# Optimization experiments

Measured on AMD Instinct MI355X. Metric: run time of the kernel, lower is better.

Reference implementation:

```python
import jax, jax.numpy as jnp
import numpy as np

T, OBS, H, NOBJ = 32768, 256, 512, 4


def _xavier(key, shape):
    fan_in, fan_out = shape[0], shape[1]
    lim = jnp.sqrt(6.0 / (fan_in + fan_out)).astype(jnp.float32)
    return jax.random.uniform(key, shape, jnp.float32, -lim, lim)


def setup_inputs() -> dict:
    key = jax.random.key(0)
    ks = jax.random.split(key, 16)
    # weights stored as [in, out] so y = x @ W (same math as nn.Linear with W.T)
    return {
        "x": jax.random.normal(ks[0], (T, OBS), jnp.float32),
        "W_in0": _xavier(ks[1], (OBS, H)),
        "W_B0": _xavier(ks[2], (OBS, H)),
        "W_C0": _xavier(ks[3], (OBS, H)),
        "W_d0": _xavier(ks[4], (OBS, H)),
        "A_log0": jax.random.normal(ks[5], (H,), jnp.float32),
        "W_in1": _xavier(ks[6], (H, H)),
        "W_B1": _xavier(ks[7], (H, H)),
        "W_C1": _xavier(ks[8], (H, H)),
        "W_d1": _xavier(ks[9], (H, H)),
        "A_log1": jax.random.normal(ks[10], (H,), jnp.float32),
        "W_out": _xavier(ks[11], (H, NOBJ)),
        "b_out": jnp.zeros((NOBJ,), jnp.float32),
        "W_skip": _xavier(ks[12], (OBS, NOBJ)),
    }


def _mamba_layer(x, W_in, W_B, W_C, W_d, A_log):
    # x: [T, D_in] -> [T, H]
    x_state = x @ W_in           # [T, H]
    B = x @ W_B                  # [T, H]
    C = x @ W_C                  # [T, H]
    delta = jax.nn.sigmoid(x @ W_d)  # [T, H]
    A = -jnp.exp(A_log)          # [H]
    A_bar = jnp.exp(delta * A)   # [T, H], in (0, 1)
    Bx = B * x_state             # [T, H]

    def step(h, inp):
        a_t, bx_t = inp
        h = a_t * h + bx_t
        return h, h

    h0 = jnp.zeros((x_state.shape[-1],), x_state.dtype)
    _, h_seq = jax.lax.scan(step, h0, (A_bar, Bx))  # [T, H]
    return C * h_seq


def reference(x, W_in0, W_B0, W_C0, W_d0, A_log0,
              W_in1, W_B1, W_C1, W_d1, A_log1,
              W_out, b_out, W_skip):
    skip = x
    y = _mamba_layer(x, W_in0, W_B0, W_C0, W_d0, A_log0)
    y = _mamba_layer(y, W_in1, W_B1, W_C1, W_d1, A_log1)
    out = y @ W_out + b_out + skip @ W_skip  # [T, NOBJ]
    return out
```

## Files before the change

### kernel.cpp

```cpp
#include <hip/hip_runtime.h>

typedef __attribute__((ext_vector_type(8))) short short8;
typedef __attribute__((ext_vector_type(4))) float floatx4;

#define T_SIZE 32768
#define OBS    256
#define H      512
#define NC     1024
#define CHUNK  32
#define NGRP   64
#define GCH    16
#define SLAB   ((size_t)T_SIZE * 32)

__device__ __forceinline__ unsigned short f2bf(float f){
    union { float f; unsigned u; } v; v.f = f;
    unsigned u = v.u;
    u += 0x7FFFu + ((u >> 16) & 1u);
    return (unsigned short)(u >> 16);
}
__device__ __forceinline__ float bf2f(unsigned short u){
    union { unsigned u; float f; } v; v.u = ((unsigned)u) << 16; return v.f;
}

#define GLOAD_LDS16(g, l) \
    __builtin_amdgcn_global_load_lds((const __attribute__((address_space(1))) unsigned*)(g), \
                                     (__attribute__((address_space(3))) unsigned*)(l), 16, 0, 0)

__global__ void cast_x_kernel(const float* __restrict__ x, unsigned short* __restrict__ xb, int n4){
    int i = blockIdx.x * 256 + threadIdx.x;
    if (i < n4){
        float4 v = ((const float4*)x)[i];
        ushort4 o;
        o.x = f2bf(v.x); o.y = f2bf(v.y); o.z = f2bf(v.z); o.w = f2bf(v.w);
        ((ushort4*)xb)[i] = o;
    }
}

__global__ void tcast4_kernel(const float* __restrict__ W0, const float* __restrict__ W1,
                              const float* __restrict__ W2, const float* __restrict__ W3,
                              unsigned short* __restrict__ dst, int K, int KH){
    int idx = blockIdx.x * 256 + threadIdx.x;
    if (idx >= 4 * KH) return;
    int s   = idx / KH;
    int rem = idx - s * KH;
    int k = rem >> 9;
    int h = rem & 511;
    const float* W = (s == 0) ? W0 : (s == 1) ? W1 : (s == 2) ? W2 : W3;
    int b = h >> 4, hh = h & 15;
    dst[(size_t)((b * 4 + s) * 16 + hh) * K + k] = f2bf(W[(size_t)k * H + h]);
}

template<int K>
__global__ __launch_bounds__(256) void gemm_layer_kernel(
    const unsigned short* __restrict__ xb,
    const unsigned short* __restrict__ wt,
    const float* __restrict__ A_log,
    unsigned short* __restrict__ gT, unsigned short* __restrict__ bxT, unsigned short* __restrict__ CT,
    float* __restrict__ Pbuf, float* __restrict__ Hbuf)
{
    __shared__ unsigned short SM[4][8192];

    const int tid  = threadIdx.x;
    const int wave = tid >> 6;
    const int lane = tid & 63;
    const int ml   = lane & 15;
    const int quad = lane >> 4;
    const int wm   = wave & 1;
    const int wn   = wave >> 1;

    const int flat = blockIdx.y * 16 + blockIdx.x;
    const int xcd  = flat & 7;
    const int j    = flat >> 3;
    const int nb   = j & 15;
    const int mb   = (j >> 4) * 8 + xcd;
    const int m0   = mb * 128;

    const int srow = tid >> 2;
    const int sel  = (((tid & 3) ^ ((tid >> 3) & 3))) * 8;
    const int swz  = (ml >> 1) & 3;

    const unsigned short* pa0 = xb + (size_t)(m0 + srow) * K + sel;
    const unsigned short* pa1 = pa0 + (size_t)64 * K;
    const unsigned short* pb0 = wt + (size_t)(nb * 128 + srow) * K + sel;
    const unsigned short* pb1 = pb0 + (size_t)64 * K;

    const int ldsA0 = (wave * 64 + 0  ) * 8;
    const int ldsA1 = (wave * 64 + 256) * 8;

    const int rbaseA = (wm * 64 + ml) * 32 + (quad ^ swz) * 8;
    const int rbaseB = (wn * 64 + ml) * 32 + (quad ^ swz) * 8;

    floatx4 acc[4][4];
    #pragma unroll
    for (int i = 0; i < 4; i++)
        #pragma unroll
        for (int jj = 0; jj < 4; jj++)
            acc[i][jj] = (floatx4)(0.0f);

    constexpr int NK = K >> 5;

    #pragma unroll
    for (int p = 0; p < 3; ++p){
        const int ko = p * 32;
        GLOAD_LDS16(pa0 + ko, &SM[p][ldsA0]);
        GLOAD_LDS16(pa1 + ko, &SM[p][ldsA1]);
        GLOAD_LDS16(pb0 + ko, &SM[p][4096 + ldsA0]);
        GLOAD_LDS16(pb1 + ko, &SM[p][4096 + ldsA1]);
    }
    asm volatile("s_waitcnt vmcnt(8)" ::: "memory");
    __builtin_amdgcn_s_barrier();
    __builtin_amdgcn_sched_barrier(0);

    #pragma unroll
    for (int kk = 0; kk < NK; ++kk){
        const int cur = kk & 3;

        if (kk + 3 < NK){
            const int ko  = (kk + 3) * 32;
            const int nb4 = (kk + 3) & 3;
            GLOAD_LDS16(pa0 + ko, &SM[nb4][ldsA0]);
            GLOAD_LDS16(pa1 + ko, &SM[nb4][ldsA1]);
            GLOAD_LDS16(pb0 + ko, &SM[nb4][4096 + ldsA0]);
            GLOAD_LDS16(pb1 + ko, &SM[nb4][4096 + ldsA1]);
        }

        short8 av[4], bv[4];
        #pragma unroll
        for (int i = 0; i < 4; i++)
            av[i] = *(const short8*)(&SM[cur][0] + rbaseA + i * 16 * 32);
        #pragma unroll
        for (int jj = 0; jj < 4; jj++)
            bv[jj] = *(const short8*)(&SM[cur][4096] + rbaseB + jj * 16 * 32);

        __builtin_amdgcn_s_setprio(1);
        #pragma unroll
        for (int i = 0; i < 4; i++)
            #pragma unroll
            for (int jj = 0; jj < 4; jj++)
                acc[i][jj] = __builtin_amdgcn_mfma_f32_16x16x32_bf16(av[i], bv[jj], acc[i][jj], 0, 0, 0);
        __builtin_amdgcn_s_setprio(0);

        if (kk + 1 < NK){
            const int hi = (kk + 3 < NK) ? (kk + 3) : (NK - 1);
            const int vm = 4 * (hi - (kk + 1));
            if (vm >= 8)      asm volatile("s_waitcnt vmcnt(8)" ::: "memory");
            else if (vm == 4) asm volatile("s_waitcnt vmcnt(4)" ::: "memory");
            else              asm volatile("s_waitcnt vmcnt(0)" ::: "memory");
            __builtin_amdgcn_s_barrier();
            __builtin_amdgcn_sched_barrier(0);
        }
    }
    __syncthreads();

    unsigned short* SMe = &SM[0][0];
    float2* segbuf = (float2*)(SMe + 12288);
    const int col = wn * 16 + ml;
    const int h   = nb * 32 + col;
    const float Aneg = -expf(A_log[h]);

    #pragma unroll
    for (int i = 0; i < 4; i++){
        float p = 1.0f, hh = 0.0f;
        #pragma unroll
        for (int r = 0; r < 4; r++){
            int trow = wm * 64 + i * 16 + quad * 4 + r;
            float dv = acc[i][3][r];
            float delta = 1.0f / (1.0f + expf(-dv));
            unsigned short gb = f2bf(delta * Aneg);
            float a = expf(bf2f(gb));
            unsigned short bb = f2bf(acc[i][1][r] * acc[i][0][r]);
            SMe[        trow * 32 + col] = gb;
            SMe[4096 +  trow * 32 + col] = bb;
            SMe[8192 +  trow * 32 + col] = f2bf(acc[i][2][r]);
            hh = fmaf(a, hh, bf2f(bb));
            p *= a;
        }
        const int ch = wm * 2 + (i >> 1);
        const int s  = (i & 1) * 4 + quad;
        segbuf[(ch * 8 + s) * 32 + col] = make_float2(p, hh);
    }
    __syncthreads();
    {
        const short8* s8 = (const short8*)SMe;
        short8* dg = (short8*)(gT  + (size_t)nb * SLAB + (size_t)m0 * 32);
        short8* db = (short8*)(bxT + (size_t)nb * SLAB + (size_t)m0 * 32);
        short8* dc = (short8*)(CT  + (size_t)nb * SLAB + (size_t)m0 * 32);
        dg[tid] = s8[tid];        dg[tid + 256] = s8[tid + 256];
        db[tid] = s8[512 + tid];  db[tid + 256] = s8[768 + tid];
        dc[tid] = s8[1024 + tid]; dc[tid + 256] = s8[1280 + tid];
    }
    if (tid < 128){
        const int ccol = tid & 31, ch = tid >> 5;
        float P = 1.0f, Hc = 0.0f;
        #pragma unroll
        for (int s = 0; s < 8; s++){
            float2 ph = segbuf[(ch * 8 + s) * 32 + ccol];
            Hc = fmaf(ph.x, Hc, ph.y);
            P *= ph.x;
        }
        const int c = mb * 4 + ch;
        Pbuf[(size_t)c * H + nb * 32 + ccol] = P;
        Hbuf[(size_t)c * H + nb * 32 + ccol] = Hc;
    }
}

__global__ void scan2a_kernel(const float* __restrict__ P, const float* __restrict__ Hc,
                              float* __restrict__ Pg, float* __restrict__ Hg){
    const int g  = blockIdx.x;
    const int j4 = threadIdx.x * 4;
    float4 pc = {1.f,1.f,1.f,1.f}, hc = {0.f,0.f,0.f,0.f};
    #pragma unroll
    for (int i = 0; i < GCH; i++){
        size_t o = (size_t)(g * GCH + i) * H + j4;
        float4 P4 = *(const float4*)(P + o);
        float4 H4 = *(const float4*)(Hc + o);
        hc.x = fmaf(P4.x, hc.x, H4.x); pc.x *= P4.x;
        hc.y = fmaf(P4.y, hc.y, H4.y); pc.y *= P4.y;
        hc.z = fmaf(P4.z, hc.z, H4.z); pc.z *= P4.z;
        hc.w = fmaf(P4.w, hc.w, H4.w); pc.w *= P4.w;
    }
    *(float4*)(Pg + (size_t)g * H + j4) = pc;
    *(float4*)(Hg + (size_t)g * H + j4) = hc;
}

__global__ void scan2b_kernel(const float* __restrict__ Pg, const float* __restrict__ Hg,
                              float* __restrict__ Cg){
    const int j = threadIdx.x;
    float carry = 0.0f;
    for (int g0 = 0; g0 < NGRP; g0 += 8){
        float p[8], h[8];
        #pragma unroll
        for (int i = 0; i < 8; i++){
            p[i] = Pg[(size_t)(g0 + i) * H + j];
            h[i] = Hg[(size_t)(g0 + i) * H + j];
        }
        #pragma unroll
        for (int i = 0; i < 8; i++){
            Cg[(size_t)(g0 + i) * H + j] = carry;
            carry = fmaf(p[i], carry, h[i]);
        }
    }
}

__global__ void scan3_kernel(const unsigned short* __restrict__ gT, const unsigned short* __restrict__ bxT,
                             const unsigned short* __restrict__ CT,
                             const float* __restrict__ P, const float* __restrict__ Hc,
                             const float* __restrict__ Cg,
                             unsigned short* __restrict__ yb){
    int idx = blockIdx.x * 256 + threadIdx.x;
    int j4 = (idx & 127) * 4;
    int c  = idx >> 7;
    int nb = j4 >> 5, jj = j4 & 31;
    int grp = c >> 4;
    float4 h = *(const float4*)(Cg + (size_t)grp * H + j4);
    for (int cc = grp << 4; cc < c; ++cc){
        float4 P4 = *(const float4*)(P + (size_t)cc * H + j4);
        float4 H4 = *(const float4*)(Hc + (size_t)cc * H + j4);
        h.x = fmaf(P4.x, h.x, H4.x);
        h.y = fmaf(P4.y, h.y, H4.y);
        h.z = fmaf(P4.z, h.z, H4.z);
        h.w = fmaf(P4.w, h.w, H4.w);
    }
    size_t off = (size_t)nb * SLAB + (size_t)c * CHUNK * 32 + jj;
    size_t yo  = (size_t)c * CHUNK * H + j4;
    #pragma unroll 8
    for (int i = 0; i < CHUNK; i++){
        ushort4 gv = *(const ushort4*)(gT + off);
        ushort4 bv = *(const ushort4*)(bxT + off);
        ushort4 cv = *(const ushort4*)(CT + off);
        h.x = fmaf(expf(bf2f(gv.x)), h.x, bf2f(bv.x));
        h.y = fmaf(expf(bf2f(gv.y)), h.y, bf2f(bv.y));
        h.z = fmaf(expf(bf2f(gv.z)), h.z, bf2f(bv.z));
        h.w = fmaf(expf(bf2f(gv.w)), h.w, bf2f(bv.w));
        ushort4 o;
        o.x = f2bf(bf2f(cv.x) * h.x);
        o.y = f2bf(bf2f(cv.y) * h.y);
        o.z = f2bf(bf2f(cv.z) * h.z);
        o.w = f2bf(bf2f(cv.w) * h.w);
        *(ushort4*)(yb + yo) = o;
        off += 32; yo += H;
    }
}

__global__ __launch_bounds__(256) void final_kernel(const unsigned short* __restrict__ y2,
                                                    const unsigned short* __restrict__ xb,
                                                    const float* __restrict__ Wout,
                                                    const float* __restrict__ bout,
                                                    const float* __restrict__ Wskip,
                                                    float* __restrict__ out){
    int wave = threadIdx.x >> 6;
    int lane = threadIdx.x & 63;
    int t = blockIdx.x * 4 + wave;
    float s0 = 0.f, s1 = 0.f, s2 = 0.f, s3 = 0.f;
    const float4* W4 = (const float4*)Wout;
    #pragma unroll
    for (int k = lane; k < H; k += 64){
        float yv = bf2f(y2[(size_t)t * H + k]);
        float4 w = W4[k];
        s0 = fmaf(yv, w.x, s0); s1 = fmaf(yv, w.y, s1);
        s2 = fmaf(yv, w.z, s2); s3 = fmaf(yv, w.w, s3);
    }
    const float4* S4 = (const float4*)Wskip;
    #pragma unroll
    for (int k = lane; k < OBS; k += 64){
        float xv = bf2f(xb[(size_t)t * OBS + k]);
        float4 w = S4[k];
        s0 = fmaf(xv, w.x, s0); s1 = fmaf(xv, w.y, s1);
        s2 = fmaf(xv, w.z, s2); s3 = fmaf(xv, w.w, s3);
    }
    #pragma unroll
    for (int off = 32; off > 0; off >>= 1){
        s0 += __shfl_down(s0, off);
        s1 += __shfl_down(s1, off);
        s2 += __shfl_down(s2, off);
        s3 += __shfl_down(s3, off);
    }
    if (lane == 0){
        out[(size_t)t * 4 + 0] = s0 + bout[0];
        out[(size_t)t * 4 + 1] = s1 + bout[1];
        out[(size_t)t * 4 + 2] = s2 + bout[2];
        out[(size_t)t * 4 + 3] = s3 + bout[3];
    }
}

extern "C" void kernel_launch(void* const* d_in, const int* in_sizes, int n_in,
                              void* d_out, int out_size, void* d_ws, size_t ws_size,
                              hipStream_t stream)
{
    const float* x     = (const float*)d_in[0];
    const float* W_in0 = (const float*)d_in[1];
    const float* W_B0  = (const float*)d_in[2];
    const float* W_C0  = (const float*)d_in[3];
    const float* W_d0  = (const float*)d_in[4];
    const float* A0    = (const float*)d_in[5];
    const float* W_in1 = (const float*)d_in[6];
    const float* W_B1  = (const float*)d_in[7];
    const float* W_C1  = (const float*)d_in[8];
    const float* W_d1  = (const float*)d_in[9];
    const float* A1    = (const float*)d_in[10];
    const float* Wout  = (const float*)d_in[11];
    const float* bout  = (const float*)d_in[12];
    const float* Wskip = (const float*)d_in[13];
    float* out = (float*)d_out;

    char* ws = (char*)d_ws;
    size_t off = 0;
    auto alloc = [&](size_t bytes) -> void* {
        void* p = ws + off;
        off += (bytes + 255) & ~(size_t)255;
        return p;
    };
    unsigned short* xb  = (unsigned short*)alloc((size_t)T_SIZE * OBS * 2);
    unsigned short* yb  = (unsigned short*)alloc((size_t)T_SIZE * H * 2);
    unsigned short* Wt0 = (unsigned short*)alloc((size_t)4 * H * OBS * 2);
    unsigned short* Wt1 = (unsigned short*)alloc((size_t)4 * H * H * 2);
    unsigned short* gT  = (unsigned short*)alloc((size_t)T_SIZE * H * 2);
    unsigned short* bxT = (unsigned short*)alloc((size_t)T_SIZE * H * 2);
    unsigned short* CT  = (unsigned short*)alloc((size_t)T_SIZE * H * 2);
    float* Pbuf = (float*)alloc((size_t)NC * H * 4);
    float* Hbuf = (float*)alloc((size_t)NC * H * 4);
    float* Pg   = (float*)alloc((size_t)NGRP * H * 4);
    float* Hg   = (float*)alloc((size_t)NGRP * H * 4);
    float* Cg   = (float*)alloc((size_t)NGRP * H * 4);
    (void)ws_size; (void)in_sizes; (void)n_in; (void)out_size;

    cast_x_kernel<<<(T_SIZE * OBS / 4 + 255) / 256, 256, 0, stream>>>(x, xb, T_SIZE * OBS / 4);
    tcast4_kernel<<<(4 * OBS * H + 255) / 256, 256, 0, stream>>>(W_in0, W_B0, W_C0, W_d0, Wt0, OBS, OBS * H);
    tcast4_kernel<<<(4 * H   * H + 255) / 256, 256, 0, stream>>>(W_in1, W_B1, W_C1, W_d1, Wt1, H,   H * H);

    dim3 ggrid(16, 256);
    const int sgrid = NC * 128 / 256;

    gemm_layer_kernel<OBS><<<ggrid, 256, 0, stream>>>(xb, Wt0, A0, gT, bxT, CT, Pbuf, Hbuf);
    scan2a_kernel<<<NGRP, 128, 0, stream>>>(Pbuf, Hbuf, Pg, Hg);
    scan2b_kernel<<<1, H, 0, stream>>>(Pg, Hg, Cg);
    scan3_kernel<<<sgrid, 256, 0, stream>>>(gT, bxT, CT, Pbuf, Hbuf, Cg, yb);

    gemm_layer_kernel<H><<<ggrid, 256, 0, stream>>>(yb, Wt1, A1, gT, bxT, CT, Pbuf, Hbuf);
    scan2a_kernel<<<NGRP, 128, 0, stream>>>(Pbuf, Hbuf, Pg, Hg);
    scan2b_kernel<<<1, H, 0, stream>>>(Pg, Hg, Cg);
    scan3_kernel<<<sgrid, 256, 0, stream>>>(gT, bxT, CT, Pbuf, Hbuf, Cg, yb );

    final_kernel<<<T_SIZE / 4, 256, 0, stream>>>(yb, xb, Wout, bout, Wskip, out);
}
```

Baseline: 334.2 us.

## Enlarge GEMM tile to 256x256 with 8 waves and split-phase prefetch

Doubles the fused projection GEMM block tile from 128x128 to 256x256 using 512 threads. Each wave now computes 128x64, and each K-step is split into two MFMA halves, with the A and B prefetches for the stage three steps ahead interleaved between the halves. The goal is more operand reuse per byte loaded and fewer blocks. The epilogue is reworked so one block writes two 32-column slabs and eight chunk summaries. The trade-off is 128 KB of shared memory and more accumulator registers, which limits occupancy, plus extra barriers per K-step.

```diff
diff --git a/kernel.cpp b/kernel.cpp
--- a/kernel.cpp
+++ b/kernel.cpp
@@ -51,156 +51,176 @@
 }
 
 template<int K>
-__global__ __launch_bounds__(256) void gemm_layer_kernel(
+__global__ __launch_bounds__(512, 2) void gemm_layer_kernel(
     const unsigned short* __restrict__ xb,
     const unsigned short* __restrict__ wt,
     const float* __restrict__ A_log,
     unsigned short* __restrict__ gT, unsigned short* __restrict__ bxT, unsigned short* __restrict__ CT,
     float* __restrict__ Pbuf, float* __restrict__ Hbuf)
 {
-    __shared__ unsigned short SM[4][8192];
+    __shared__ unsigned short SM[4][16384];
 
     const int tid  = threadIdx.x;
     const int wave = tid >> 6;
     const int lane = tid & 63;
     const int ml   = lane & 15;
     const int quad = lane >> 4;
-    const int wm   = wave & 1;
-    const int wn   = wave >> 1;
-
-    const int flat = blockIdx.y * 16 + blockIdx.x;
+    const int wm   = wave >> 2;
+    const int wn   = wave & 3;
+
+    const int flat = blockIdx.y * 8 + blockIdx.x;
     const int xcd  = flat & 7;
     const int j    = flat >> 3;
-    const int nb   = j & 15;
-    const int mb   = (j >> 4) * 8 + xcd;
-    const int m0   = mb * 128;
+    const int nb   = j & 7;
+    const int mb   = (j >> 3) * 8 + xcd;
+    const int m0   = mb * 256;
 
     const int srow = tid >> 2;
-    const int sel  = (((tid & 3) ^ ((tid >> 3) & 3))) * 8;
+    const int sel  = ((tid & 3) ^ ((tid >> 3) & 3)) * 8;
     const int swz  = (ml >> 1) & 3;
 
     const unsigned short* pa0 = xb + (size_t)(m0 + srow) * K + sel;
-    const unsigned short* pa1 = pa0 + (size_t)64 * K;
-    const unsigned short* pb0 = wt + (size_t)(nb * 128 + srow) * K + sel;
-    const unsigned short* pb1 = pb0 + (size_t)64 * K;
-
-    const int ldsA0 = (wave * 64 + 0  ) * 8;
-    const int ldsA1 = (wave * 64 + 256) * 8;
-
-    const int rbaseA = (wm * 64 + ml) * 32 + (quad ^ swz) * 8;
-    const int rbaseB = (wn * 64 + ml) * 32 + (quad ^ swz) * 8;
-
-    floatx4 acc[4][4];
-    #pragma unroll
-    for (int i = 0; i < 4; i++)
-        #pragma unroll
-        for (int jj = 0; jj < 4; jj++)
-            acc[i][jj] = (floatx4)(0.0f);
+    const unsigned short* pa1 = pa0 + (size_t)128 * K;
+    const unsigned short* pb0 = wt + (size_t)(nb * 256 + srow) * K + sel;
+    const unsigned short* pb1 = pb0 + (size_t)128 * K;
+
+    const int ldsA0 = wave * 512;
+    const int ldsA1 = 4096  + wave * 512;
+    const int ldsB0 = 8192  + wave * 512;
+    const int ldsB1 = 12288 + wave * 512;
+
+    const int rbaseA = (wm * 128 + ml) * 32 + (quad ^ swz) * 8;
+    const int rbaseB = (wn * 64  + ml) * 32 + (quad ^ swz) * 8;
+
+    floatx4 acc[8][4];
+    #pragma unroll
+    for (int m = 0; m < 8; m++)
+        #pragma unroll
+        for (int n = 0; n < 4; n++)
+            acc[m][n] = (floatx4)(0.0f);
 
     constexpr int NK = K >> 5;
 
-    #pragma unroll
-    for (int p = 0; p < 3; ++p){
-        const int ko = p * 32;
-        GLOAD_LDS16(pa0 + ko, &SM[p][ldsA0]);
-        GLOAD_LDS16(pa1 + ko, &SM[p][ldsA1]);
-        GLOAD_LDS16(pb0 + ko, &SM[p][4096 + ldsA0]);
-        GLOAD_LDS16(pb1 + ko, &SM[p][4096 + ldsA1]);
-    }
+#define STAGE_A(kt_) { const int b_ = (kt_) & 3; const int ko_ = (kt_) * 32; \
+        GLOAD_LDS16(pa0 + ko_, &SM[b_][ldsA0]); \
+        GLOAD_LDS16(pa1 + ko_, &SM[b_][ldsA1]); }
+#define STAGE_B(kt_) { const int b_ = (kt_) & 3; const int ko_ = (kt_) * 32; \
+        GLOAD_LDS16(pb0 + ko_, &SM[b_][ldsB0]); \
+        GLOAD_LDS16(pb1 + ko_, &SM[b_][ldsB1]); }
+
+    STAGE_A(0); STAGE_B(0);
+    STAGE_A(1); STAGE_B(1);
+    STAGE_A(2); STAGE_B(2);
     asm volatile("s_waitcnt vmcnt(8)" ::: "memory");
     __builtin_amdgcn_s_barrier();
     __builtin_amdgcn_sched_barrier(0);
 
     #pragma unroll
-    for (int kk = 0; kk < NK; ++kk){
-        const int cur = kk & 3;
-
-        if (kk + 3 < NK){
-            const int ko  = (kk + 3) * 32;
-            const int nb4 = (kk + 3) & 3;
-            GLOAD_LDS16(pa0 + ko, &SM[nb4][ldsA0]);
-            GLOAD_LDS16(pa1 + ko, &SM[nb4][ldsA1]);
-            GLOAD_LDS16(pb0 + ko, &SM[nb4][4096 + ldsA0]);
-            GLOAD_LDS16(pb1 + ko, &SM[nb4][4096 + ldsA1]);
-        }
+    for (int kt = 0; kt < NK; ++kt){
+        const unsigned short* SA = &SM[kt & 3][0];
+        const unsigned short* SB = SA + 8192;
 
         short8 av[4], bv[4];
         #pragma unroll
-        for (int i = 0; i < 4; i++)
-            av[i] = *(const short8*)(&SM[cur][0] + rbaseA + i * 16 * 32);
-        #pragma unroll
-        for (int jj = 0; jj < 4; jj++)
-            bv[jj] = *(const short8*)(&SM[cur][4096] + rbaseB + jj * 16 * 32);
-
+        for (int m = 0; m < 4; m++) av[m] = *(const short8*)(SA + rbaseA + m * 512);
+        #pragma unroll
+        for (int n = 0; n < 4; n++) bv[n] = *(const short8*)(SB + rbaseB + n * 512);
+        if (kt + 3 < NK) STAGE_A(kt + 3);
+        __builtin_amdgcn_s_barrier();
+        asm volatile("s_waitcnt lgkmcnt(0)" ::: "memory");
+        __builtin_amdgcn_sched_barrier(0);
         __builtin_amdgcn_s_setprio(1);
         #pragma unroll
-        for (int i = 0; i < 4; i++)
+        for (int m = 0; m < 4; m++)
             #pragma unroll
-            for (int jj = 0; jj < 4; jj++)
-                acc[i][jj] = __builtin_amdgcn_mfma_f32_16x16x32_bf16(av[i], bv[jj], acc[i][jj], 0, 0, 0);
+            for (int n = 0; n < 4; n++)
+                acc[m][n] = __builtin_amdgcn_mfma_f32_16x16x32_bf16(av[m], bv[n], acc[m][n], 0, 0, 0);
         __builtin_amdgcn_s_setprio(0);
-
-        if (kk + 1 < NK){
-            const int hi = (kk + 3 < NK) ? (kk + 3) : (NK - 1);
-            const int vm = 4 * (hi - (kk + 1));
-            if (vm >= 8)      asm volatile("s_waitcnt vmcnt(8)" ::: "memory");
-            else if (vm == 4) asm volatile("s_waitcnt vmcnt(4)" ::: "memory");
-            else              asm volatile("s_waitcnt vmcnt(0)" ::: "memory");
-            __builtin_amdgcn_s_barrier();
-            __builtin_amdgcn_sched_barrier(0);
-        }
+        __builtin_amdgcn_s_barrier();
+        __builtin_amdgcn_sched_barrier(0);
+
+        short8 aw[4];
+        #pragma unroll
+        for (int m = 0; m < 4; m++) aw[m] = *(const short8*)(SA + rbaseA + (m + 4) * 512);
+        if (kt + 3 < NK) STAGE_B(kt + 3);
+        __builtin_amdgcn_s_barrier();
+        asm volatile("s_waitcnt lgkmcnt(0)" ::: "memory");
+        __builtin_amdgcn_sched_barrier(0);
+        __builtin_amdgcn_s_setprio(1);
+        #pragma unroll
+        for (int m = 0; m < 4; m++)
+            #pragma unroll
+            for (int n = 0; n < 4; n++)
+                acc[m + 4][n] = __builtin_amdgcn_mfma_f32_16x16x32_bf16(aw[m], bv[n], acc[m + 4][n], 0, 0, 0);
+        __builtin_amdgcn_s_setprio(0);
+        if (kt + 1 < NK){
+            if (kt + 3 < NK)       { asm volatile("s_waitcnt vmcnt(8)" ::: "memory"); }
+            else if (kt + 3 == NK) { asm volatile("s_waitcnt vmcnt(4)" ::: "memory"); }
+            else                   { asm volatile("s_waitcnt vmcnt(0)" ::: "memory"); }
+        }
+        __builtin_amdgcn_s_barrier();
+        __builtin_amdgcn_sched_barrier(0);
     }
     __syncthreads();
 
+#undef STAGE_A
+#undef STAGE_B
+
     unsigned short* SMe = &SM[0][0];
-    float2* segbuf = (float2*)(SMe + 12288);
-    const int col = wn * 16 + ml;
-    const int h   = nb * 32 + col;
-    const float Aneg = -expf(A_log[h]);
-
-    #pragma unroll
-    for (int i = 0; i < 4; i++){
+    float2* segbuf = (float2*)(SMe + 49152);
+    const int hcol  = wn * 16 + ml;
+    const int hb    = wn >> 1;
+    const int col32 = (wn & 1) * 16 + ml;
+    const float Aneg = -expf(A_log[(nb * 4 + wn) * 16 + ml]);
+
+    #pragma unroll
+    for (int m = 0; m < 8; m++){
         float p = 1.0f, hh = 0.0f;
         #pragma unroll
         for (int r = 0; r < 4; r++){
-            int trow = wm * 64 + i * 16 + quad * 4 + r;
-            float dv = acc[i][3][r];
+            int trow = wm * 128 + m * 16 + quad * 4 + r;
+            float dv = acc[m][3][r];
             float delta = 1.0f / (1.0f + expf(-dv));
             unsigned short gb = f2bf(delta * Aneg);
             float a = expf(bf2f(gb));
-            unsigned short bb = f2bf(acc[i][1][r] * acc[i][0][r]);
-            SMe[        trow * 32 + col] = gb;
-            SMe[4096 +  trow * 32 + col] = bb;
-            SMe[8192 +  trow * 32 + col] = f2bf(acc[i][2][r]);
+            unsigned short bb = f2bf(acc[m][1][r] * acc[m][0][r]);
+            int base = hb * 8192 + trow * 32 + col32;
+            SMe[        base] = gb;
+            SMe[16384 + base] = bb;
+            SMe[32768 + base] = f2bf(acc[m][2][r]);
             hh = fmaf(a, hh, bf2f(bb));
             p *= a;
         }
-        const int ch = wm * 2 + (i >> 1);
-        const int s  = (i & 1) * 4 + quad;
-        segbuf[(ch * 8 + s) * 32 + col] = make_float2(p, hh);
+        const int ch = wm * 4 + (m >> 1);
+        const int s  = (m & 1) * 4 + quad;
+        segbuf[(ch * 8 + s) * 64 + hcol] = make_float2(p, hh);
     }
     __syncthreads();
     {
         const short8* s8 = (const short8*)SMe;
-        short8* dg = (short8*)(gT  + (size_t)nb * SLAB + (size_t)m0 * 32);
-        short8* db = (short8*)(bxT + (size_t)nb * SLAB + (size_t)m0 * 32);
-        short8* dc = (short8*)(CT  + (size_t)nb * SLAB + (size_t)m0 * 32);
-        dg[tid] = s8[tid];        dg[tid + 256] = s8[tid + 256];
-        db[tid] = s8[512 + tid];  db[tid + 256] = s8[768 + tid];
-        dc[tid] = s8[1024 + tid]; dc[tid + 256] = s8[1280 + tid];
-    }
-    if (tid < 128){
-        const int ccol = tid & 31, ch = tid >> 5;
+        #pragma unroll
+        for (int arr = 0; arr < 3; arr++){
+            unsigned short* bp = (arr == 0) ? gT : (arr == 1) ? bxT : CT;
+            #pragma unroll
+            for (int h2 = 0; h2 < 2; h2++){
+                short8* d = (short8*)(bp + (size_t)(nb * 2 + h2) * SLAB + (size_t)m0 * 32);
+                d[tid]       = s8[arr * 2048 + h2 * 1024 + tid];
+                d[tid + 512] = s8[arr * 2048 + h2 * 1024 + tid + 512];
+            }
+        }
+    }
+    {
+        const int ccol = tid & 63, ch = tid >> 6;
         float P = 1.0f, Hc = 0.0f;
         #pragma unroll
         for (int s = 0; s < 8; s++){
-            float2 ph = segbuf[(ch * 8 + s) * 32 + ccol];
+            float2 ph = segbuf[(ch * 8 + s) * 64 + ccol];
             Hc = fmaf(ph.x, Hc, ph.y);
             P *= ph.x;
         }
-        const int c = mb * 4 + ch;
-        Pbuf[(size_t)c * H + nb * 32 + ccol] = P;
-        Hbuf[(size_t)c * H + nb * 32 + ccol] = Hc;
+        const int c = mb * 8 + ch;
+        Pbuf[(size_t)c * H + nb * 64 + ccol] = P;
+        Hbuf[(size_t)c * H + nb * 64 + ccol] = Hc;
     }
 }
 
@@ -368,15 +388,15 @@
     tcast4_kernel<<<(4 * OBS * H + 255) / 256, 256, 0, stream>>>(W_in0, W_B0, W_C0, W_d0, Wt0, OBS, OBS * H);
     tcast4_kernel<<<(4 * H   * H + 255) / 256, 256, 0, stream>>>(W_in1, W_B1, W_C1, W_d1, Wt1, H,   H * H);
 
-    dim3 ggrid(16, 256);
+    dim3 ggrid(8, 128);
     const int sgrid = NC * 128 / 256;
 
-    gemm_layer_kernel<OBS><<<ggrid, 256, 0, stream>>>(xb, Wt0, A0, gT, bxT, CT, Pbuf, Hbuf);
+    gemm_layer_kernel<OBS><<<ggrid, 512, 0, stream>>>(xb, Wt0, A0, gT, bxT, CT, Pbuf, Hbuf);
     scan2a_kernel<<<NGRP, 128, 0, stream>>>(Pbuf, Hbuf, Pg, Hg);
     scan2b_kernel<<<1, H, 0, stream>>>(Pg, Hg, Cg);
     scan3_kernel<<<sgrid, 256, 0, stream>>>(gT, bxT, CT, Pbuf, Hbuf, Cg, yb);
 
-    gemm_layer_kernel<H><<<ggrid, 256, 0, stream>>>(yb, Wt1, A1, gT, bxT, CT, Pbuf, Hbuf);
+    gemm_layer_kernel<H><<<ggrid, 512, 0, stream>>>(yb, Wt1, A1, gT, bxT, CT, Pbuf, Hbuf);
     scan2a_kernel<<<NGRP, 128, 0, stream>>>(Pbuf, Hbuf, Pg, Hg);
     scan2b_kernel<<<1, H, 0, stream>>>(Pg, Hg, Cg);
     scan3_kernel<<<sgrid, 256, 0, stream>>>(gT, bxT, CT, Pbuf, Hbuf, Cg, yb );
```

Result: no change. 336.0 us (+0.6%).

## Fuse prep casts, drop group-carry scan kernel, fuse final projection into scan

Applied to the files above, without the earlier changes.

Merges the x cast and both weight transpose-casts into one prep launch. Removes the serial single-block scan2b kernel by having each scan3 thread recompute its group carry from the group prefix arrays, which costs up to 63 extra float4 steps per thread. The last layer's scan is fused with the output projection: each block stages its 64 output rows in LDS (64 KB) and computes the 4-wide dot products directly, so the second-layer y buffer is never written to or read back from global memory. That shared-memory use may cut occupancy for the fused kernel.

```diff
diff --git a/kernel.cpp b/kernel.cpp
--- a/kernel.cpp
+++ b/kernel.cpp
@@ -26,28 +26,42 @@
     __builtin_amdgcn_global_load_lds((const __attribute__((address_space(1))) unsigned*)(g), \
                                      (__attribute__((address_space(3))) unsigned*)(l), 16, 0, 0)
 
-__global__ void cast_x_kernel(const float* __restrict__ x, unsigned short* __restrict__ xb, int n4){
-    int i = blockIdx.x * 256 + threadIdx.x;
-    if (i < n4){
+__global__ void prep_kernel(const float* __restrict__ x, unsigned short* __restrict__ xb,
+                            const float* __restrict__ A0W0, const float* __restrict__ A0W1,
+                            const float* __restrict__ A0W2, const float* __restrict__ A0W3,
+                            unsigned short* __restrict__ Wt0,
+                            const float* __restrict__ A1W0, const float* __restrict__ A1W1,
+                            const float* __restrict__ A1W2, const float* __restrict__ A1W3,
+                            unsigned short* __restrict__ Wt1){
+    const int b = blockIdx.x;
+    const int tid = threadIdx.x;
+    if (b < 8192){
+        int i = b * 256 + tid;
         float4 v = ((const float4*)x)[i];
         ushort4 o;
         o.x = f2bf(v.x); o.y = f2bf(v.y); o.z = f2bf(v.z); o.w = f2bf(v.w);
         ((ushort4*)xb)[i] = o;
-    }
-}
-
-__global__ void tcast4_kernel(const float* __restrict__ W0, const float* __restrict__ W1,
-                              const float* __restrict__ W2, const float* __restrict__ W3,
-                              unsigned short* __restrict__ dst, int K, int KH){
-    int idx = blockIdx.x * 256 + threadIdx.x;
-    if (idx >= 4 * KH) return;
-    int s   = idx / KH;
-    int rem = idx - s * KH;
-    int k = rem >> 9;
-    int h = rem & 511;
-    const float* W = (s == 0) ? W0 : (s == 1) ? W1 : (s == 2) ? W2 : W3;
-    int b = h >> 4, hh = h & 15;
-    dst[(size_t)((b * 4 + s) * 16 + hh) * K + k] = f2bf(W[(size_t)k * H + h]);
+    } else if (b < 10240){
+        const int K = OBS, KH = OBS * H;
+        int idx = (b - 8192) * 256 + tid;
+        int s   = idx / KH;
+        int rem = idx - s * KH;
+        int k = rem >> 9;
+        int h = rem & 511;
+        const float* W = (s == 0) ? A0W0 : (s == 1) ? A0W1 : (s == 2) ? A0W2 : A0W3;
+        int bb = h >> 4, hh = h & 15;
+        Wt0[(size_t)((bb * 4 + s) * 16 + hh) * K + k] = f2bf(W[(size_t)k * H + h]);
+    } else {
+        const int K = H, KH = H * H;
+        int idx = (b - 10240) * 256 + tid;
+        int s   = idx / KH;
+        int rem = idx - s * KH;
+        int k = rem >> 9;
+        int h = rem & 511;
+        const float* W = (s == 0) ? A1W0 : (s == 1) ? A1W1 : (s == 2) ? A1W2 : A1W3;
+        int bb = h >> 4, hh = h & 15;
+        Wt1[(size_t)((bb * 4 + s) * 16 + hh) * K + k] = f2bf(W[(size_t)k * H + h]);
+    }
 }
 
 template<int K>
@@ -223,36 +237,25 @@
     *(float4*)(Hg + (size_t)g * H + j4) = hc;
 }
 
-__global__ void scan2b_kernel(const float* __restrict__ Pg, const float* __restrict__ Hg,
-                              float* __restrict__ Cg){
-    const int j = threadIdx.x;
-    float carry = 0.0f;
-    for (int g0 = 0; g0 < NGRP; g0 += 8){
-        float p[8], h[8];
-        #pragma unroll
-        for (int i = 0; i < 8; i++){
-            p[i] = Pg[(size_t)(g0 + i) * H + j];
-            h[i] = Hg[(size_t)(g0 + i) * H + j];
-        }
-        #pragma unroll
-        for (int i = 0; i < 8; i++){
-            Cg[(size_t)(g0 + i) * H + j] = carry;
-            carry = fmaf(p[i], carry, h[i]);
-        }
-    }
-}
-
 __global__ void scan3_kernel(const unsigned short* __restrict__ gT, const unsigned short* __restrict__ bxT,
                              const unsigned short* __restrict__ CT,
                              const float* __restrict__ P, const float* __restrict__ Hc,
-                             const float* __restrict__ Cg,
+                             const float* __restrict__ Pg, const float* __restrict__ Hg,
                              unsigned short* __restrict__ yb){
     int idx = blockIdx.x * 256 + threadIdx.x;
     int j4 = (idx & 127) * 4;
     int c  = idx >> 7;
     int nb = j4 >> 5, jj = j4 & 31;
     int grp = c >> 4;
-    float4 h = *(const float4*)(Cg + (size_t)grp * H + j4);
+    float4 h = {0.f, 0.f, 0.f, 0.f};
+    for (int g = 0; g < grp; ++g){
+        float4 P4 = *(const float4*)(Pg + (size_t)g * H + j4);
+        float4 H4 = *(const float4*)(Hg + (size_t)g * H + j4);
+        h.x = fmaf(P4.x, h.x, H4.x);
+        h.y = fmaf(P4.y, h.y, H4.y);
+        h.z = fmaf(P4.z, h.z, H4.z);
+        h.w = fmaf(P4.w, h.w, H4.w);
+    }
     for (int cc = grp << 4; cc < c; ++cc){
         float4 P4 = *(const float4*)(P + (size_t)cc * H + j4);
         float4 H4 = *(const float4*)(Hc + (size_t)cc * H + j4);
@@ -282,44 +285,96 @@
     }
 }
 
-__global__ __launch_bounds__(256) void final_kernel(const unsigned short* __restrict__ y2,
-                                                    const unsigned short* __restrict__ xb,
-                                                    const float* __restrict__ Wout,
-                                                    const float* __restrict__ bout,
-                                                    const float* __restrict__ Wskip,
-                                                    float* __restrict__ out){
-    int wave = threadIdx.x >> 6;
-    int lane = threadIdx.x & 63;
-    int t = blockIdx.x * 4 + wave;
-    float s0 = 0.f, s1 = 0.f, s2 = 0.f, s3 = 0.f;
+__global__ __launch_bounds__(256) void scan3f_kernel(
+    const unsigned short* __restrict__ gT, const unsigned short* __restrict__ bxT,
+    const unsigned short* __restrict__ CT,
+    const float* __restrict__ P, const float* __restrict__ Hc,
+    const float* __restrict__ Pg, const float* __restrict__ Hg,
+    const unsigned short* __restrict__ xb,
+    const float* __restrict__ Wout, const float* __restrict__ bout,
+    const float* __restrict__ Wskip,
+    float* __restrict__ out){
+    __shared__ unsigned short ystage[64 * 512];
+    const int tid = threadIdx.x;
+    int idx = blockIdx.x * 256 + tid;
+    int j4 = (idx & 127) * 4;
+    int c  = idx >> 7;
+    int nb = j4 >> 5, jj = j4 & 31;
+    int grp = c >> 4;
+    float4 h = {0.f, 0.f, 0.f, 0.f};
+    for (int g = 0; g < grp; ++g){
+        float4 P4 = *(const float4*)(Pg + (size_t)g * H + j4);
+        float4 H4 = *(const float4*)(Hg + (size_t)g * H + j4);
+        h.x = fmaf(P4.x, h.x, H4.x);
+        h.y = fmaf(P4.y, h.y, H4.y);
+        h.z = fmaf(P4.z, h.z, H4.z);
+        h.w = fmaf(P4.w, h.w, H4.w);
+    }
+    for (int cc = grp << 4; cc < c; ++cc){
+        float4 P4 = *(const float4*)(P + (size_t)cc * H + j4);
+        float4 H4 = *(const float4*)(Hc + (size_t)cc * H + j4);
+        h.x = fmaf(P4.x, h.x, H4.x);
+        h.y = fmaf(P4.y, h.y, H4.y);
+        h.z = fmaf(P4.z, h.z, H4.z);
+        h.w = fmaf(P4.w, h.w, H4.w);
+    }
+    size_t off = (size_t)nb * SLAB + (size_t)c * CHUNK * 32 + jj;
+    const int lrow = (tid >> 7) * 32;
+    #pragma unroll 8
+    for (int i = 0; i < CHUNK; i++){
+        ushort4 gv = *(const ushort4*)(gT + off);
+        ushort4 bv = *(const ushort4*)(bxT + off);
+        ushort4 cv = *(const ushort4*)(CT + off);
+        h.x = fmaf(expf(bf2f(gv.x)), h.x, bf2f(bv.x));
+        h.y = fmaf(expf(bf2f(gv.y)), h.y, bf2f(bv.y));
+        h.z = fmaf(expf(bf2f(gv.z)), h.z, bf2f(bv.z));
+        h.w = fmaf(expf(bf2f(gv.w)), h.w, bf2f(bv.w));
+        ushort4 o;
+        o.x = f2bf(bf2f(cv.x) * h.x);
+        o.y = f2bf(bf2f(cv.y) * h.y);
+        o.z = f2bf(bf2f(cv.z) * h.z);
+        o.w = f2bf(bf2f(cv.w) * h.w);
+        *(ushort4*)(&ystage[(lrow + i) * 512 + j4]) = o;
+        off += 32;
+    }
+    __syncthreads();
+
+    const int wave = tid >> 6;
+    const int lane = tid & 63;
     const float4* W4 = (const float4*)Wout;
-    #pragma unroll
-    for (int k = lane; k < H; k += 64){
-        float yv = bf2f(y2[(size_t)t * H + k]);
-        float4 w = W4[k];
-        s0 = fmaf(yv, w.x, s0); s1 = fmaf(yv, w.y, s1);
-        s2 = fmaf(yv, w.z, s2); s3 = fmaf(yv, w.w, s3);
-    }
     const float4* S4 = (const float4*)Wskip;
-    #pragma unroll
-    for (int k = lane; k < OBS; k += 64){
-        float xv = bf2f(xb[(size_t)t * OBS + k]);
-        float4 w = S4[k];
-        s0 = fmaf(xv, w.x, s0); s1 = fmaf(xv, w.y, s1);
-        s2 = fmaf(xv, w.z, s2); s3 = fmaf(xv, w.w, s3);
-    }
-    #pragma unroll
-    for (int off = 32; off > 0; off >>= 1){
-        s0 += __shfl_down(s0, off);
-        s1 += __shfl_down(s1, off);
-        s2 += __shfl_down(s2, off);
-        s3 += __shfl_down(s3, off);
-    }
-    if (lane == 0){
-        out[(size_t)t * 4 + 0] = s0 + bout[0];
-        out[(size_t)t * 4 + 1] = s1 + bout[1];
-        out[(size_t)t * 4 + 2] = s2 + bout[2];
-        out[(size_t)t * 4 + 3] = s3 + bout[3];
+    const float b0 = bout[0], b1 = bout[1], b2 = bout[2], b3 = bout[3];
+    for (int rr = 0; rr < 16; ++rr){
+        const int r = wave * 16 + rr;
+        const int t = blockIdx.x * 64 + r;
+        float s0 = 0.f, s1 = 0.f, s2 = 0.f, s3 = 0.f;
+        #pragma unroll
+        for (int k = lane; k < H; k += 64){
+            float yv = bf2f(ystage[r * 512 + k]);
+            float4 w = W4[k];
+            s0 = fmaf(yv, w.x, s0); s1 = fmaf(yv, w.y, s1);
+            s2 = fmaf(yv, w.z, s2); s3 = fmaf(yv, w.w, s3);
+        }
+        #pragma unroll
+        for (int k = lane; k < OBS; k += 64){
+            float xv = bf2f(xb[(size_t)t * OBS + k]);
+            float4 w = S4[k];
+            s0 = fmaf(xv, w.x, s0); s1 = fmaf(xv, w.y, s1);
+            s2 = fmaf(xv, w.z, s2); s3 = fmaf(xv, w.w, s3);
+        }
+        #pragma unroll
+        for (int o = 32; o > 0; o >>= 1){
+            s0 += __shfl_down(s0, o);
+            s1 += __shfl_down(s1, o);
+            s2 += __shfl_down(s2, o);
+            s3 += __shfl_down(s3, o);
+        }
+        if (lane == 0){
+            out[(size_t)t * 4 + 0] = s0 + b0;
+            out[(size_t)t * 4 + 1] = s1 + b1;
+            out[(size_t)t * 4 + 2] = s2 + b2;
+            out[(size_t)t * 4 + 3] = s3 + b3;
+        }
     }
 }
 
@@ -361,25 +416,21 @@
     float* Hbuf = (float*)alloc((size_t)NC * H * 4);
     float* Pg   = (float*)alloc((size_t)NGRP * H * 4);
     float* Hg   = (float*)alloc((size_t)NGRP * H * 4);
-    float* Cg   = (float*)alloc((size_t)NGRP * H * 4);
     (void)ws_size; (void)in_sizes; (void)n_in; (void)out_size;
 
-    cast_x_kernel<<<(T_SIZE * OBS / 4 + 255) / 256, 256, 0, stream>>>(x, xb, T_SIZE * OBS / 4);
-    tcast4_kernel<<<(4 * OBS * H + 255) / 256, 256, 0, stream>>>(W_in0, W_B0, W_C0, W_d0, Wt0, OBS, OBS * H);
-    tcast4_kernel<<<(4 * H   * H + 255) / 256, 256, 0, stream>>>(W_in1, W_B1, W_C1, W_d1, Wt1, H,   H * H);
+    prep_kernel<<<14336, 256, 0, stream>>>(x, xb,
+                                           W_in0, W_B0, W_C0, W_d0, Wt0,
+                                           W_in1, W_B1, W_C1, W_d1, Wt1);
 
     dim3 ggrid(16, 256);
     const int sgrid = NC * 128 / 256;
 
     gemm_layer_kernel<OBS><<<ggrid, 256, 0, stream>>>(xb, Wt0, A0, gT, bxT, CT, Pbuf, Hbuf);
     scan2a_kernel<<<NGRP, 128, 0, stream>>>(Pbuf, Hbuf, Pg, Hg);
-    scan2b_kernel<<<1, H, 0, stream>>>(Pg, Hg, Cg);
-    scan3_kernel<<<sgrid, 256, 0, stream>>>(gT, bxT, CT, Pbuf, Hbuf, Cg, yb);
+    scan3_kernel<<<sgrid, 256, 0, stream>>>(gT, bxT, CT, Pbuf, Hbuf, Pg, Hg, yb);
 
     gemm_layer_kernel<H><<<ggrid, 256, 0, stream>>>(yb, Wt1, A1, gT, bxT, CT, Pbuf, Hbuf);
     scan2a_kernel<<<NGRP, 128, 0, stream>>>(Pbuf, Hbuf, Pg, Hg);
-    scan2b_kernel<<<1, H, 0, stream>>>(Pg, Hg, Cg);
-    scan3_kernel<<<sgrid, 256, 0, stream>>>(gT, bxT, CT, Pbuf, Hbuf, Cg, yb );
-
-    final_kernel<<<T_SIZE / 4, 256, 0, stream>>>(yb, xb, Wout, bout, Wskip, out);
-}
+    scan3f_kernel<<<sgrid, 256, 0, stream>>>(gT, bxT, CT, Pbuf, Hbuf, Pg, Hg,
+                                             xb, Wout, bout, Wskip, out);
+}
```

Measured after the change: 328.3 us. About the same (-1.8%).
